# Kernel tuning notes

Measured on AMD Instinct MI355X. Metric: run time of the kernel, lower is better.

Reference implementation:

```python
import jax, jax.numpy as jnp
import numpy as np

N, D_IN, D_OUT = 8192, 1024, 1024

def setup_inputs() -> dict:
    key = jax.random.key(0)
    k1, k2, k3, k4 = jax.random.split(key, 4)
    scale = 1.0 / np.sqrt(D_IN).astype(np.float32)
    return {
        "X": jax.random.normal(k1, (N, D_IN), dtype=jnp.float32),
        "W_Q": jax.random.normal(k2, (D_IN, D_OUT), dtype=jnp.float32) * scale,
        "W_K": jax.random.normal(k3, (D_IN, D_OUT), dtype=jnp.float32) * scale,
        "W_V": jax.random.normal(k4, (D_IN, D_OUT), dtype=jnp.float32) * scale,
    }

def reference(X, W_Q, W_K, W_V):
    # Manual single-head self-attention over the N rows of X.
    Q = X @ W_Q            # [N, d_out]
    Kmat = X @ W_K         # [N, d_out]
    V = X @ W_V            # [N, d_out]
    inv_sqrt_d = jnp.asarray(1.0 / np.sqrt(W_Q.shape[1]), dtype=Q.dtype)
    scores = (Q @ Kmat.T) * inv_sqrt_d            # [N, N]
    attn = jax.nn.softmax(scores, axis=-1)        # row-wise softmax (Keras default axis=-1)
    return attn @ V                               # [N, d_out]
```

## Files before the change

kernel.cpp:

```cpp
#include <hip/hip_runtime.h>

#define N_ROWS 8192
#define D_DIM  1024
#define SM_SHIFT 4.0f

typedef _Float16 f16;
typedef _Float16 f16x8 __attribute__((ext_vector_type(8)));
typedef _Float16 f16x4 __attribute__((ext_vector_type(4)));
typedef float    f32x4 __attribute__((ext_vector_type(4)));

__device__ __forceinline__ void gload16(const void* g, void* l) {
  __builtin_amdgcn_global_load_lds(
      (const __attribute__((address_space(1))) void*)g,
      (__attribute__((address_space(3))) void*)l, 16, 0, 0);
}

__device__ __forceinline__ int xcd_swz(int bid, int nb) {
  return (bid & 7) * (nb >> 3) + (bid >> 3);
}

__device__ __forceinline__ void tile2d4(int bid, int ny_t, int& nx, int& ny) {
  const int v = xcd_swz(bid, 32 * ny_t);
  const int g = v >> 4, w = v & 15;
  const int gpc = ny_t >> 2;
  const int gx = g / gpc, gy = g - gx * gpc;
  nx = gx * 4 + (w & 3);
  ny = gy * 4 + (w >> 2);
}

__global__ __launch_bounds__(256) void f32_to_f16_kernel(
    const float* __restrict__ in, f16* __restrict__ out, int n4) {
  for (int i = blockIdx.x * blockDim.x + threadIdx.x; i < n4;
       i += gridDim.x * blockDim.x) {
    float4 x = ((const float4*)in)[i];
    f16x4 h = {(f16)x.x, (f16)x.y, (f16)x.z, (f16)x.w};
    ((f16x4*)out)[i] = h;
  }
}

__global__ __launch_bounds__(256) void transpose_w_kernel(
    const float* __restrict__ w0, const float* __restrict__ w1,
    const float* __restrict__ w2, f16* __restrict__ WT) {
  const float* W = (blockIdx.z == 0) ? w0 : (blockIdx.z == 1) ? w1 : w2;
  f16* T = WT + (size_t)blockIdx.z * D_DIM * D_DIM;
  __shared__ float tile[64][65];
  const int r0 = blockIdx.y * 64, c0 = blockIdx.x * 64;
  const int t = threadIdx.x;
#pragma unroll
  for (int rep = 0; rep < 16; ++rep) {
    int idx = rep * 256 + t;
    int r = idx >> 6, c = idx & 63;
    tile[r][c] = W[(size_t)(r0 + r) * D_DIM + (c0 + c)];
  }
  __syncthreads();
#pragma unroll
  for (int rep = 0; rep < 16; ++rep) {
    int idx = rep * 256 + t;
    int r = idx >> 6, c = idx & 63;
    T[(size_t)(c0 + r) * D_DIM + (r0 + c)] = (f16)tile[c][r];
  }
}

template <bool SWAP>
__device__ __forceinline__ void mainloop256(const f16* __restrict__ Ag, int lda,
                                            const f16* __restrict__ Bg,
                                            int ldbt, int nk, f16* LA, f16* LB,
                                            f32x4 (&acc)[8][4], int tid) {
  const int lane = tid & 63;
  const int wr = tid >> 8, wc = (tid >> 6) & 3;
  const int ro = lane & 15;
  const int jj0 = (((lane >> 4) ^ (ro & 7)) << 4);
  const int rs = tid >> 3;
  const int ce = ((tid & 7) ^ (rs & 7)) * 8;
  const f16* a[4];
  const f16* b[4];
#pragma unroll
  for (int s = 0; s < 4; ++s) {
    a[s] = Ag + (size_t)(rs + 64 * s) * lda + ce;
    b[s] = Bg + (size_t)(rs + 64 * s) * ldbt + ce;
  }
  char* la = (char*)LA;
  char* lb = (char*)LB;
  const int t16 = tid * 16;

  auto stage = [&](int buf) {
    char* A = la + buf * 32768;
    char* B = lb + buf * 32768;
#pragma unroll
    for (int s = 0; s < 4; ++s) {
      gload16(a[s], A + s * 8192 + t16);
      gload16(b[s], B + s * 8192 + t16);
    }
#pragma unroll
    for (int s = 0; s < 4; ++s) {
      a[s] += 64;
      b[s] += 64;
    }
  };

  stage(0);

  for (int kt = 0; kt < nk; ++kt) {
    const int buf = kt & 1;
    if (kt + 1 < nk) {
      stage(buf ^ 1);
      asm volatile("s_waitcnt vmcnt(8)" ::: "memory");
    } else {
      asm volatile("s_waitcnt vmcnt(0)" ::: "memory");
    }
    __builtin_amdgcn_s_barrier();
    __builtin_amdgcn_sched_barrier(0);
    const char* ab = la + buf * 32768;
    const char* bb = lb + buf * 32768;
#pragma unroll
    for (int h = 0; h < 2; ++h) {
      const int jo = jj0 ^ (h << 6);
      f16x8 af[8], bf[4];
#pragma unroll
      for (int mi = 0; mi < 8; ++mi)
        af[mi] = *(const f16x8*)(ab + (wr * 128 + mi * 16 + ro) * 128 + jo);
#pragma unroll
      for (int ni = 0; ni < 4; ++ni)
        bf[ni] = *(const f16x8*)(bb + (wc * 64 + ni * 16 + ro) * 128 + jo);
      asm volatile("s_waitcnt lgkmcnt(0)" ::: "memory");
      __builtin_amdgcn_sched_barrier(0);
      __builtin_amdgcn_s_setprio(1);
#pragma unroll
      for (int mi = 0; mi < 8; ++mi)
#pragma unroll
        for (int ni = 0; ni < 4; ++ni)
          acc[mi][ni] =
              SWAP ? __builtin_amdgcn_mfma_f32_16x16x32_f16(
                         bf[ni], af[mi], acc[mi][ni], 0, 0, 0)
                   : __builtin_amdgcn_mfma_f32_16x16x32_f16(
                         af[mi], bf[ni], acc[mi][ni], 0, 0, 0);
      __builtin_amdgcn_s_setprio(0);
    }
    __builtin_amdgcn_s_barrier();
  }
}

#define ACC_INIT8(acc)                                \
  _Pragma("unroll") for (int i = 0; i < 8; ++i)       \
      _Pragma("unroll") for (int j = 0; j < 4; ++j)   \
          acc[i][j] = (f32x4){0.f, 0.f, 0.f, 0.f};

__global__ __launch_bounds__(512, 2) void gemm_qkv(
    const f16* __restrict__ Xh, const f16* __restrict__ WT,
    f16* __restrict__ Q, f16* __restrict__ Kh, f16* __restrict__ VT) {
  __shared__ f16 LA[2][16384], LB[2][16384];
  const int v = xcd_swz(blockIdx.x, 384);
  const int z = v >> 7, r = v & 127;
  const int nx = r & 3, ny = r >> 2;
  const int tid = threadIdx.x, lane = tid & 63;
  const int wr = tid >> 8, wc = (tid >> 6) & 3;
  const int ro = lane & 15, rq = (lane >> 4) * 4;

  const f16* A = Xh + (size_t)ny * 256 * D_DIM;
  const f16* B = WT + (size_t)z * D_DIM * D_DIM + (size_t)nx * 256 * D_DIM;

  f32x4 acc[8][4];
  ACC_INIT8(acc);
  if (z < 2) {
    mainloop256<true>(A, D_DIM, B, D_DIM, D_DIM / 64, &LA[0][0], &LB[0][0],
                      acc, tid);
    f16* C = z ? Kh : Q;
#pragma unroll
    for (int mi = 0; mi < 8; ++mi) {
      const size_t xr = ny * 256 + wr * 128 + mi * 16 + ro;
#pragma unroll
      for (int ni = 0; ni < 4; ++ni) {
        f16x4 pk;
#pragma unroll
        for (int rr = 0; rr < 4; ++rr) pk[rr] = (f16)acc[mi][ni][rr];
        *(f16x4*)&C[xr * D_DIM + nx * 256 + wc * 64 + ni * 16 + rq] = pk;
      }
    }
  } else {
    mainloop256<false>(A, D_DIM, B, D_DIM, D_DIM / 64, &LA[0][0], &LB[0][0],
                       acc, tid);
#pragma unroll
    for (int mi = 0; mi < 8; ++mi)
#pragma unroll
      for (int ni = 0; ni < 4; ++ni) {
        f16x4 pk;
#pragma unroll
        for (int rr = 0; rr < 4; ++rr) pk[rr] = (f16)acc[mi][ni][rr];
        const size_t d = nx * 256 + wc * 64 + ni * 16 + ro;
        *(f16x4*)&VT[d * N_ROWS + ny * 256 + wr * 128 + mi * 16 + rq] = pk;
      }
  }
}

__global__ __launch_bounds__(512, 2) void gemm_s_exp(
    const f16* __restrict__ Q, const f16* __restrict__ Kh, f16* __restrict__ S,
    float* __restrict__ Lpart, int nyb) {
  __shared__ f16 LA[2][16384], LB[2][16384];
  int nx, ny;
  tile2d4(blockIdx.x, nyb, nx, ny);
  const int tid = threadIdx.x, lane = tid & 63;
  const int wr = tid >> 8, wc = (tid >> 6) & 3;
  const int ro = lane & 15, rq = (lane >> 4) * 4;

  f32x4 acc[8][4];
  ACC_INIT8(acc);
  mainloop256<true>(Q + (size_t)ny * 256 * D_DIM, D_DIM,
                    Kh + (size_t)nx * 256 * D_DIM, D_DIM, D_DIM / 64,
                    &LA[0][0], &LB[0][0], acc, tid);

  const float sc = 0.03125f;
#pragma unroll
  for (int mi = 0; mi < 8; ++mi) {
    const size_t q = ny * 256 + wr * 128 + mi * 16 + ro;
    f16* srow = S + q * N_ROWS + nx * 256 + wc * 64 + rq;
    float rs = 0.f;
#pragma unroll
    for (int ni = 0; ni < 4; ++ni) {
      f16x4 pk;
#pragma unroll
      for (int rr = 0; rr < 4; ++rr) {
        const float p = __expf(acc[mi][ni][rr] * sc - SM_SHIFT);
        rs += p;
        pk[rr] = (f16)p;
      }
      *(f16x4*)&srow[ni * 16] = pk;
    }
    rs += __shfl_xor(rs, 16, 64);
    rs += __shfl_xor(rs, 32, 64);
    if (lane < 16) Lpart[q * 128 + nx * 4 + wc] = rs;
  }
}

__global__ __launch_bounds__(256) void reduce_l(const float* __restrict__ Lpart,
                                                float* __restrict__ linv,
                                                int rows) {
  const int w = (blockIdx.x * 256 + threadIdx.x) >> 6;
  const int lane = threadIdx.x & 63;
  if (w >= rows) return;
  const float* p = Lpart + (size_t)w * 128;
  float s = p[lane] + p[lane + 64];
#pragma unroll
  for (int o = 32; o > 0; o >>= 1) s += __shfl_xor(s, o, 64);
  if (lane == 0) linv[w] = 1.0f / s;
}

__global__ __launch_bounds__(512, 2) void gemm_pv(const f16* __restrict__ S,
                                                  const f16* __restrict__ VT,
                                                  float* __restrict__ Ppart,
                                                  int nyb, int KS, int chunk) {
  __shared__ f16 LA[2][16384], LB[2][16384];
  const int nid = xcd_swz(blockIdx.x, (int)gridDim.x);
  const int nx = nid & 3, ny = (nid >> 2) % nyb, z = (nid >> 2) / nyb;
  const int tid = threadIdx.x, lane = tid & 63;
  const int wr = tid >> 8, wc = (tid >> 6) & 3;
  const int ro = lane & 15, rq = (lane >> 4) * 4;

  f32x4 acc[8][4];
  ACC_INIT8(acc);
  mainloop256<true>(S + (size_t)ny * 256 * N_ROWS + (size_t)z * KS, N_ROWS,
                    VT + (size_t)nx * 256 * N_ROWS + (size_t)z * KS, N_ROWS,
                    KS / 64, &LA[0][0], &LB[0][0], acc, tid);

  float* out = Ppart + (size_t)z * chunk * D_DIM;
#pragma unroll
  for (int mi = 0; mi < 8; ++mi) {
    const size_t q = ny * 256 + wr * 128 + mi * 16 + ro;
#pragma unroll
    for (int ni = 0; ni < 4; ++ni)
      *(f32x4*)&out[q * D_DIM + nx * 256 + wc * 64 + ni * 16 + rq] =
          acc[mi][ni];
  }
}

__global__ __launch_bounds__(256) void reduce_o(
    const float* __restrict__ Ppart, const float* __restrict__ linv,
    float* __restrict__ O, int rows, int sk) {
  const int n4 = rows * 256;
  const int stride = gridDim.x * blockDim.x;
  for (int i = blockIdx.x * 256 + threadIdx.x; i < n4; i += stride) {
    f32x4 s = ((const f32x4*)Ppart)[i];
    for (int t = 1; t < sk; ++t) s += ((const f32x4*)Ppart)[(size_t)t * n4 + i];
    const float il = linv[i >> 8];
    ((f32x4*)O)[i] = s * il;
  }
}

extern "C" void kernel_launch(void* const* d_in, const int* in_sizes, int n_in,
                              void* d_out, int out_size, void* d_ws,
                              size_t ws_size, hipStream_t stream) {
  (void)in_sizes;
  (void)n_in;
  (void)out_size;
  const float* X = (const float*)d_in[0];
  const float* WQ = (const float*)d_in[1];
  const float* WK = (const float*)d_in[2];
  const float* WV = (const float*)d_in[3];
  float* O = (float*)d_out;

  const size_t fixedA = (size_t)N_ROWS * D_DIM * 2 + 3ull * D_DIM * D_DIM * 2;
  int chunk = 1024, sk = 1;
  const int pref[][2] = {{8192, 2}, {4096, 2}, {2048, 2}, {8192, 1},
                         {4096, 1}, {2048, 1}, {1024, 1}};
  for (int i = 0; i < 7; ++i) {
    const int c = pref[i][0], s = pref[i][1];
    size_t R = (size_t)s * c * D_DIM * 4;
    if (R < fixedA) R = fixedA;
    const size_t need = R + 3ull * N_ROWS * D_DIM * 2 + (size_t)c * N_ROWS * 2 +
                        (size_t)c * 128 * 4 + (size_t)c * 4 + 4096;
    if (need <= ws_size) {
      chunk = c;
      sk = s;
      break;
    }
  }

  char* base = (char*)d_ws;
  f16* Xh = (f16*)base;
  f16* WT = (f16*)(base + (size_t)N_ROWS * D_DIM * 2);
  float* Ppart = (float*)base;
  size_t R = (size_t)sk * chunk * D_DIM * 4;
  if (R < fixedA) R = fixedA;
  char* p = base + ((R + 255) & ~(size_t)255);
  f16* Q = (f16*)p;
  p += (size_t)N_ROWS * D_DIM * 2;
  f16* Kh = (f16*)p;
  p += (size_t)N_ROWS * D_DIM * 2;
  f16* VT = (f16*)p;
  p += (size_t)N_ROWS * D_DIM * 2;
  f16* S = (f16*)p;
  p += (size_t)chunk * N_ROWS * 2;
  float* Lpart = (float*)p;
  p += (size_t)chunk * 128 * 4;
  float* linv = (float*)p;

  f32_to_f16_kernel<<<2048, 256, 0, stream>>>(X, Xh, N_ROWS * D_DIM / 4);
  transpose_w_kernel<<<dim3(16, 16, 3), 256, 0, stream>>>(WQ, WK, WV, WT);
  gemm_qkv<<<384, 512, 0, stream>>>(Xh, WT, Q, Kh, VT);

  const int KS = N_ROWS / sk;
  for (int mc = 0; mc < N_ROWS; mc += chunk) {
    const int nyb = chunk / 256;
    gemm_s_exp<<<32 * nyb, 512, 0, stream>>>(Q + (size_t)mc * D_DIM, Kh, S,
                                             Lpart, nyb);
    reduce_l<<<(chunk + 3) / 4, 256, 0, stream>>>(Lpart, linv, chunk);
    gemm_pv<<<4 * nyb * sk, 512, 0, stream>>>(S, VT, Ppart, nyb, KS, chunk);
    reduce_o<<<1024, 256, 0, stream>>>(Ppart, linv, O + (size_t)mc * D_DIM,
                                       chunk, sk);
  }
}
```

Before: 403.0 us.

## Restructure GEMM mainloop into four barriered phases with prefetch-after-compute staging

Splits each K-tile of the shared GEMM mainloop into four phases. Each phase loads half of the A fragments, plus B when it is needed, then issues 16 MFMAs with a workgroup barrier in between, in the style of ping-pong scheduling. Both buffers are staged up front, and the next global-to-LDS load into the buffer just consumed is issued only after all its compute finishes. This holds fewer fragments in registers and interleaves waves more tightly. In exchange it adds more barriers per tile and delays the prefetch issue, which reduces load/compute overlap.

```diff
diff --git a/kernel.cpp b/kernel.cpp
--- a/kernel.cpp
+++ b/kernel.cpp
@@ -98,46 +98,72 @@
     }
   };
 
+  f16x8 af[4], bf[4];
+  auto readA = [&](const char* ab, int h, int jo) {
+#pragma unroll
+    for (int j = 0; j < 4; ++j)
+      af[j] = *(const f16x8*)(ab + (wr * 128 + h * 64 + j * 16 + ro) * 128 + jo);
+  };
+  auto readB = [&](const char* bb, int jo) {
+#pragma unroll
+    for (int ni = 0; ni < 4; ++ni)
+      bf[ni] = *(const f16x8*)(bb + (wc * 64 + ni * 16 + ro) * 128 + jo);
+  };
+
+#define PHASE_TAIL(H)                                                     \
+  __builtin_amdgcn_s_barrier();                                           \
+  __builtin_amdgcn_sched_barrier(0);                                      \
+  asm volatile("s_waitcnt lgkmcnt(0)" ::: "memory");                      \
+  __builtin_amdgcn_sched_barrier(0);                                      \
+  __builtin_amdgcn_s_setprio(1);                                          \
+  _Pragma("unroll") for (int j = 0; j < 4; ++j)                           \
+  _Pragma("unroll") for (int ni = 0; ni < 4; ++ni)                        \
+      acc[(H) * 4 + j][ni] =                                              \
+          SWAP ? __builtin_amdgcn_mfma_f32_16x16x32_f16(bf[ni], af[j],    \
+                                                        acc[(H) * 4 + j][ni], \
+                                                        0, 0, 0)          \
+               : __builtin_amdgcn_mfma_f32_16x16x32_f16(af[j], bf[ni],    \
+                                                        acc[(H) * 4 + j][ni], \
+                                                        0, 0, 0);         \
+  __builtin_amdgcn_s_setprio(0);
+
   stage(0);
+  if (nk > 1) {
+    stage(1);
+    asm volatile("s_waitcnt vmcnt(8)" ::: "memory");
+  } else {
+    asm volatile("s_waitcnt vmcnt(0)" ::: "memory");
+  }
+  __builtin_amdgcn_s_barrier();
+  __builtin_amdgcn_sched_barrier(0);
 
   for (int kt = 0; kt < nk; ++kt) {
     const int buf = kt & 1;
-    if (kt + 1 < nk) {
-      stage(buf ^ 1);
-      asm volatile("s_waitcnt vmcnt(8)" ::: "memory");
-    } else {
-      asm volatile("s_waitcnt vmcnt(0)" ::: "memory");
-    }
+    const char* ab = la + buf * 32768;
+    const char* bb = lb + buf * 32768;
+    readA(ab, 0, jj0);
+    readB(bb, jj0);
+    PHASE_TAIL(0)
+    readA(ab, 1, jj0);
+    PHASE_TAIL(1)
+    readA(ab, 0, jj0 ^ 64);
+    readB(bb, jj0 ^ 64);
+    PHASE_TAIL(0)
+    readA(ab, 1, jj0 ^ 64);
+    PHASE_TAIL(1)
     __builtin_amdgcn_s_barrier();
     __builtin_amdgcn_sched_barrier(0);
-    const char* ab = la + buf * 32768;
-    const char* bb = lb + buf * 32768;
-#pragma unroll
-    for (int h = 0; h < 2; ++h) {
-      const int jo = jj0 ^ (h << 6);
-      f16x8 af[8], bf[4];
-#pragma unroll
-      for (int mi = 0; mi < 8; ++mi)
-        af[mi] = *(const f16x8*)(ab + (wr * 128 + mi * 16 + ro) * 128 + jo);
-#pragma unroll
-      for (int ni = 0; ni < 4; ++ni)
-        bf[ni] = *(const f16x8*)(bb + (wc * 64 + ni * 16 + ro) * 128 + jo);
-      asm volatile("s_waitcnt lgkmcnt(0)" ::: "memory");
+    if (kt + 2 < nk) stage(buf);
+    if (kt + 1 < nk) {
+      if (kt + 2 < nk)
+        asm volatile("s_waitcnt vmcnt(8)" ::: "memory");
+      else
+        asm volatile("s_waitcnt vmcnt(0)" ::: "memory");
+      __builtin_amdgcn_s_barrier();
       __builtin_amdgcn_sched_barrier(0);
-      __builtin_amdgcn_s_setprio(1);
-#pragma unroll
-      for (int mi = 0; mi < 8; ++mi)
-#pragma unroll
-        for (int ni = 0; ni < 4; ++ni)
-          acc[mi][ni] =
-              SWAP ? __builtin_amdgcn_mfma_f32_16x16x32_f16(
-                         bf[ni], af[mi], acc[mi][ni], 0, 0, 0)
-                   : __builtin_amdgcn_mfma_f32_16x16x32_f16(
-                         af[mi], bf[ni], acc[mi][ni], 0, 0, 0);
-      __builtin_amdgcn_s_setprio(0);
-    }
-    __builtin_amdgcn_s_barrier();
-  }
+    }
+  }
+#undef PHASE_TAIL
 }
 
 #define ACC_INIT8(acc)                                \
```

Result: no change. 410.2 us (+1.8%).

## Shrink GEMM tiles to 128x256, single-buffer LDS and raise occupancy

Applied to the files above, without the earlier changes.

Replaces the 256x256 double-buffered GEMM mainloop with a 128x256 tile that uses a single LDS buffer (48KB) and launch bounds for 4 blocks per CU. LDS fragment loads are split into two k-halves, with a partial lgkmcnt wait so the first MFMA batch can start while the second half loads. Grids double to cover the smaller M tiles. The aim is to hide memory latency through more resident blocks rather than in-block prefetch. The cost is less data reuse per tile, global loads that are no longer overlapped inside a block, and a 128-VGPR budget that may be tight for 64 accumulator registers.

```diff
diff --git a/kernel.cpp b/kernel.cpp
--- a/kernel.cpp
+++ b/kernel.cpp
@@ -61,158 +61,166 @@
   }
 }
 
-template <bool SWAP>
-__device__ __forceinline__ void mainloop256(const f16* __restrict__ Ag, int lda,
-                                            const f16* __restrict__ Bg,
-                                            int ldbt, int nk, f16* LA, f16* LB,
-                                            f32x4 (&acc)[8][4], int tid) {
+template <bool SWAP, int LDA, int LDB>
+__device__ __forceinline__ void mainloop(const f16* __restrict__ Ag,
+                                         const f16* __restrict__ Bg, int nk,
+                                         f16* LA, f16* LB, f32x4 (&acc)[4][4],
+                                         int tid) {
   const int lane = tid & 63;
-  const int wr = tid >> 8, wc = (tid >> 6) & 3;
+  const int wm = tid >> 8;
+  const int wn = (tid >> 6) & 3;
   const int ro = lane & 15;
   const int jj0 = (((lane >> 4) ^ (ro & 7)) << 4);
   const int rs = tid >> 3;
   const int ce = ((tid & 7) ^ (rs & 7)) * 8;
-  const f16* a[4];
-  const f16* b[4];
-#pragma unroll
-  for (int s = 0; s < 4; ++s) {
-    a[s] = Ag + (size_t)(rs + 64 * s) * lda + ce;
-    b[s] = Bg + (size_t)(rs + 64 * s) * ldbt + ce;
-  }
+  const f16* a0 = Ag + (size_t)rs * LDA + ce;
+  const f16* a1 = Ag + (size_t)(rs + 64) * LDA + ce;
+  const f16* b0 = Bg + (size_t)rs * LDB + ce;
+  const f16* b1 = Bg + (size_t)(rs + 64) * LDB + ce;
+  const f16* b2 = Bg + (size_t)(rs + 128) * LDB + ce;
+  const f16* b3 = Bg + (size_t)(rs + 192) * LDB + ce;
   char* la = (char*)LA;
   char* lb = (char*)LB;
   const int t16 = tid * 16;
 
-  auto stage = [&](int buf) {
-    char* A = la + buf * 32768;
-    char* B = lb + buf * 32768;
-#pragma unroll
-    for (int s = 0; s < 4; ++s) {
-      gload16(a[s], A + s * 8192 + t16);
-      gload16(b[s], B + s * 8192 + t16);
-    }
-#pragma unroll
-    for (int s = 0; s < 4; ++s) {
-      a[s] += 64;
-      b[s] += 64;
-    }
+  auto stage = [&]() {
+    gload16(a0, la + t16);
+    gload16(a1, la + 8192 + t16);
+    gload16(b0, lb + t16);
+    gload16(b1, lb + 8192 + t16);
+    gload16(b2, lb + 16384 + t16);
+    gload16(b3, lb + 24576 + t16);
+    a0 += 64;
+    a1 += 64;
+    b0 += 64;
+    b1 += 64;
+    b2 += 64;
+    b3 += 64;
   };
 
-  stage(0);
+  stage();
 
   for (int kt = 0; kt < nk; ++kt) {
-    const int buf = kt & 1;
-    if (kt + 1 < nk) {
-      stage(buf ^ 1);
-      asm volatile("s_waitcnt vmcnt(8)" ::: "memory");
-    } else {
-      asm volatile("s_waitcnt vmcnt(0)" ::: "memory");
-    }
+    asm volatile("s_waitcnt vmcnt(0)" ::: "memory");
     __builtin_amdgcn_s_barrier();
     __builtin_amdgcn_sched_barrier(0);
-    const char* ab = la + buf * 32768;
-    const char* bb = lb + buf * 32768;
-#pragma unroll
-    for (int h = 0; h < 2; ++h) {
-      const int jo = jj0 ^ (h << 6);
-      f16x8 af[8], bf[4];
-#pragma unroll
-      for (int mi = 0; mi < 8; ++mi)
-        af[mi] = *(const f16x8*)(ab + (wr * 128 + mi * 16 + ro) * 128 + jo);
+    const int jo0 = jj0, jo1 = jj0 ^ 64;
+    f16x8 af0[4], bf0[4], af1[4], bf1[4];
+#pragma unroll
+    for (int j = 0; j < 4; ++j)
+      af0[j] = *(const f16x8*)(la + (wm * 64 + j * 16 + ro) * 128 + jo0);
+#pragma unroll
+    for (int ni = 0; ni < 4; ++ni)
+      bf0[ni] = *(const f16x8*)(lb + (wn * 64 + ni * 16 + ro) * 128 + jo0);
+#pragma unroll
+    for (int j = 0; j < 4; ++j)
+      af1[j] = *(const f16x8*)(la + (wm * 64 + j * 16 + ro) * 128 + jo1);
+    asm volatile("s_waitcnt lgkmcnt(4)" ::: "memory");
+    __builtin_amdgcn_sched_barrier(0);
+    __builtin_amdgcn_s_setprio(1);
+#pragma unroll
+    for (int j = 0; j < 4; ++j)
 #pragma unroll
       for (int ni = 0; ni < 4; ++ni)
-        bf[ni] = *(const f16x8*)(bb + (wc * 64 + ni * 16 + ro) * 128 + jo);
-      asm volatile("s_waitcnt lgkmcnt(0)" ::: "memory");
-      __builtin_amdgcn_sched_barrier(0);
-      __builtin_amdgcn_s_setprio(1);
-#pragma unroll
-      for (int mi = 0; mi < 8; ++mi)
-#pragma unroll
-        for (int ni = 0; ni < 4; ++ni)
-          acc[mi][ni] =
-              SWAP ? __builtin_amdgcn_mfma_f32_16x16x32_f16(
-                         bf[ni], af[mi], acc[mi][ni], 0, 0, 0)
-                   : __builtin_amdgcn_mfma_f32_16x16x32_f16(
-                         af[mi], bf[ni], acc[mi][ni], 0, 0, 0);
-      __builtin_amdgcn_s_setprio(0);
-    }
+        acc[j][ni] =
+            SWAP ? __builtin_amdgcn_mfma_f32_16x16x32_f16(bf0[ni], af0[j],
+                                                          acc[j][ni], 0, 0, 0)
+                 : __builtin_amdgcn_mfma_f32_16x16x32_f16(af0[j], bf0[ni],
+                                                          acc[j][ni], 0, 0, 0);
+    __builtin_amdgcn_s_setprio(0);
+#pragma unroll
+    for (int ni = 0; ni < 4; ++ni)
+      bf1[ni] = *(const f16x8*)(lb + (wn * 64 + ni * 16 + ro) * 128 + jo1);
+    asm volatile("s_waitcnt lgkmcnt(0)" ::: "memory");
+    __builtin_amdgcn_sched_barrier(0);
+    __builtin_amdgcn_s_setprio(1);
+#pragma unroll
+    for (int j = 0; j < 4; ++j)
+#pragma unroll
+      for (int ni = 0; ni < 4; ++ni)
+        acc[j][ni] =
+            SWAP ? __builtin_amdgcn_mfma_f32_16x16x32_f16(bf1[ni], af1[j],
+                                                          acc[j][ni], 0, 0, 0)
+                 : __builtin_amdgcn_mfma_f32_16x16x32_f16(af1[j], bf1[ni],
+                                                          acc[j][ni], 0, 0, 0);
+    __builtin_amdgcn_s_setprio(0);
     __builtin_amdgcn_s_barrier();
-  }
-}
-
-#define ACC_INIT8(acc)                                \
-  _Pragma("unroll") for (int i = 0; i < 8; ++i)       \
+    __builtin_amdgcn_sched_barrier(0);
+    if (kt + 1 < nk) stage();
+  }
+}
+
+#define ACC_INIT4(acc)                                \
+  _Pragma("unroll") for (int i = 0; i < 4; ++i)       \
       _Pragma("unroll") for (int j = 0; j < 4; ++j)   \
           acc[i][j] = (f32x4){0.f, 0.f, 0.f, 0.f};
 
-__global__ __launch_bounds__(512, 2) void gemm_qkv(
+__global__ __launch_bounds__(512, 4) void gemm_qkv(
     const f16* __restrict__ Xh, const f16* __restrict__ WT,
     f16* __restrict__ Q, f16* __restrict__ Kh, f16* __restrict__ VT) {
-  __shared__ f16 LA[2][16384], LB[2][16384];
-  const int v = xcd_swz(blockIdx.x, 384);
-  const int z = v >> 7, r = v & 127;
+  __shared__ f16 LA[8192], LB[16384];
+  const int v = xcd_swz(blockIdx.x, 768);
+  const int z = v >> 8, r = v & 255;
   const int nx = r & 3, ny = r >> 2;
   const int tid = threadIdx.x, lane = tid & 63;
-  const int wr = tid >> 8, wc = (tid >> 6) & 3;
+  const int wm = tid >> 8, wn = (tid >> 6) & 3;
   const int ro = lane & 15, rq = (lane >> 4) * 4;
 
-  const f16* A = Xh + (size_t)ny * 256 * D_DIM;
+  const f16* A = Xh + (size_t)ny * 128 * D_DIM;
   const f16* B = WT + (size_t)z * D_DIM * D_DIM + (size_t)nx * 256 * D_DIM;
 
-  f32x4 acc[8][4];
-  ACC_INIT8(acc);
+  f32x4 acc[4][4];
+  ACC_INIT4(acc);
   if (z < 2) {
-    mainloop256<true>(A, D_DIM, B, D_DIM, D_DIM / 64, &LA[0][0], &LB[0][0],
-                      acc, tid);
+    mainloop<true, D_DIM, D_DIM>(A, B, D_DIM / 64, LA, LB, acc, tid);
     f16* C = z ? Kh : Q;
 #pragma unroll
-    for (int mi = 0; mi < 8; ++mi) {
-      const size_t xr = ny * 256 + wr * 128 + mi * 16 + ro;
+    for (int mi = 0; mi < 4; ++mi) {
+      const size_t xr = ny * 128 + wm * 64 + mi * 16 + ro;
 #pragma unroll
       for (int ni = 0; ni < 4; ++ni) {
         f16x4 pk;
 #pragma unroll
         for (int rr = 0; rr < 4; ++rr) pk[rr] = (f16)acc[mi][ni][rr];
-        *(f16x4*)&C[xr * D_DIM + nx * 256 + wc * 64 + ni * 16 + rq] = pk;
+        *(f16x4*)&C[xr * D_DIM + nx * 256 + wn * 64 + ni * 16 + rq] = pk;
       }
     }
   } else {
-    mainloop256<false>(A, D_DIM, B, D_DIM, D_DIM / 64, &LA[0][0], &LB[0][0],
-                       acc, tid);
-#pragma unroll
-    for (int mi = 0; mi < 8; ++mi)
+    mainloop<false, D_DIM, D_DIM>(A, B, D_DIM / 64, LA, LB, acc, tid);
+#pragma unroll
+    for (int mi = 0; mi < 4; ++mi)
 #pragma unroll
       for (int ni = 0; ni < 4; ++ni) {
         f16x4 pk;
 #pragma unroll
         for (int rr = 0; rr < 4; ++rr) pk[rr] = (f16)acc[mi][ni][rr];
-        const size_t d = nx * 256 + wc * 64 + ni * 16 + ro;
-        *(f16x4*)&VT[d * N_ROWS + ny * 256 + wr * 128 + mi * 16 + rq] = pk;
+        const size_t d = nx * 256 + wn * 64 + ni * 16 + ro;
+        *(f16x4*)&VT[d * N_ROWS + ny * 128 + wm * 64 + mi * 16 + rq] = pk;
       }
   }
 }
 
-__global__ __launch_bounds__(512, 2) void gemm_s_exp(
+__global__ __launch_bounds__(512, 4) void gemm_s_exp(
     const f16* __restrict__ Q, const f16* __restrict__ Kh, f16* __restrict__ S,
     float* __restrict__ Lpart, int nyb) {
-  __shared__ f16 LA[2][16384], LB[2][16384];
+  __shared__ f16 LA[8192], LB[16384];
   int nx, ny;
   tile2d4(blockIdx.x, nyb, nx, ny);
   const int tid = threadIdx.x, lane = tid & 63;
-  const int wr = tid >> 8, wc = (tid >> 6) & 3;
+  const int wm = tid >> 8, wn = (tid >> 6) & 3;
   const int ro = lane & 15, rq = (lane >> 4) * 4;
 
-  f32x4 acc[8][4];
-  ACC_INIT8(acc);
-  mainloop256<true>(Q + (size_t)ny * 256 * D_DIM, D_DIM,
-                    Kh + (size_t)nx * 256 * D_DIM, D_DIM, D_DIM / 64,
-                    &LA[0][0], &LB[0][0], acc, tid);
+  f32x4 acc[4][4];
+  ACC_INIT4(acc);
+  mainloop<true, D_DIM, D_DIM>(Q + (size_t)ny * 128 * D_DIM,
+                               Kh + (size_t)nx * 256 * D_DIM, D_DIM / 64, LA,
+                               LB, acc, tid);
 
   const float sc = 0.03125f;
 #pragma unroll
-  for (int mi = 0; mi < 8; ++mi) {
-    const size_t q = ny * 256 + wr * 128 + mi * 16 + ro;
-    f16* srow = S + q * N_ROWS + nx * 256 + wc * 64 + rq;
+  for (int mi = 0; mi < 4; ++mi) {
+    const size_t q = ny * 128 + wm * 64 + mi * 16 + ro;
+    f16* srow = S + q * N_ROWS + nx * 256 + wn * 64 + rq;
     float rs = 0.f;
 #pragma unroll
     for (int ni = 0; ni < 4; ++ni) {
@@ -227,7 +235,7 @@
     }
     rs += __shfl_xor(rs, 16, 64);
     rs += __shfl_xor(rs, 32, 64);
-    if (lane < 16) Lpart[q * 128 + nx * 4 + wc] = rs;
+    if (lane < 16) Lpart[q * 128 + nx * 4 + wn] = rs;
   }
 }
 
@@ -244,30 +252,31 @@
   if (lane == 0) linv[w] = 1.0f / s;
 }
 
-__global__ __launch_bounds__(512, 2) void gemm_pv(const f16* __restrict__ S,
+__global__ __launch_bounds__(512, 4) void gemm_pv(const f16* __restrict__ S,
                                                   const f16* __restrict__ VT,
                                                   float* __restrict__ Ppart,
                                                   int nyb, int KS, int chunk) {
-  __shared__ f16 LA[2][16384], LB[2][16384];
+  __shared__ f16 LA[8192], LB[16384];
   const int nid = xcd_swz(blockIdx.x, (int)gridDim.x);
   const int nx = nid & 3, ny = (nid >> 2) % nyb, z = (nid >> 2) / nyb;
   const int tid = threadIdx.x, lane = tid & 63;
-  const int wr = tid >> 8, wc = (tid >> 6) & 3;
+  const int wm = tid >> 8, wn = (tid >> 6) & 3;
   const int ro = lane & 15, rq = (lane >> 4) * 4;
 
-  f32x4 acc[8][4];
-  ACC_INIT8(acc);
-  mainloop256<true>(S + (size_t)ny * 256 * N_ROWS + (size_t)z * KS, N_ROWS,
-                    VT + (size_t)nx * 256 * N_ROWS + (size_t)z * KS, N_ROWS,
-                    KS / 64, &LA[0][0], &LB[0][0], acc, tid);
+  f32x4 acc[4][4];
+  ACC_INIT4(acc);
+  mainloop<true, N_ROWS, N_ROWS>(S + (size_t)ny * 128 * N_ROWS + (size_t)z * KS,
+                                 VT + (size_t)nx * 256 * N_ROWS +
+                                     (size_t)z * KS,
+                                 KS / 64, LA, LB, acc, tid);
 
   float* out = Ppart + (size_t)z * chunk * D_DIM;
 #pragma unroll
-  for (int mi = 0; mi < 8; ++mi) {
-    const size_t q = ny * 256 + wr * 128 + mi * 16 + ro;
+  for (int mi = 0; mi < 4; ++mi) {
+    const size_t q = ny * 128 + wm * 64 + mi * 16 + ro;
 #pragma unroll
     for (int ni = 0; ni < 4; ++ni)
-      *(f32x4*)&out[q * D_DIM + nx * 256 + wc * 64 + ni * 16 + rq] =
+      *(f32x4*)&out[q * D_DIM + nx * 256 + wn * 64 + ni * 16 + rq] =
           acc[mi][ni];
   }
 }
@@ -335,11 +344,11 @@
 
   f32_to_f16_kernel<<<2048, 256, 0, stream>>>(X, Xh, N_ROWS * D_DIM / 4);
   transpose_w_kernel<<<dim3(16, 16, 3), 256, 0, stream>>>(WQ, WK, WV, WT);
-  gemm_qkv<<<384, 512, 0, stream>>>(Xh, WT, Q, Kh, VT);
+  gemm_qkv<<<768, 512, 0, stream>>>(Xh, WT, Q, Kh, VT);
 
   const int KS = N_ROWS / sk;
   for (int mc = 0; mc < N_ROWS; mc += chunk) {
-    const int nyb = chunk / 256;
+    const int nyb = chunk / 128;
     gemm_s_exp<<<32 * nyb, 512, 0, stream>>>(Q + (size_t)mc * D_DIM, Kh, S,
                                              Lpart, nyb);
     reduce_l<<<(chunk + 3) / 4, 256, 0, stream>>>(Lpart, linv, chunk);
```

Result: slower. 496.9 us (+23.3%).
